# Kernel tuning notes

Measured on AMD Instinct MI355X. Metric: run time of the kernel, lower is better.

The kernel has to match this reference:

```python
import jax, jax.numpy as jnp
import numpy as np

B, S, EMB, H = 2, 2048, 1024, 16
D = EMB // H  # per-head dim = 64
SCALE = 1.0 / np.sqrt(D).astype(np.float32)


def setup_inputs() -> dict:
    key = jax.random.key(0)
    ks = jax.random.split(key, 11)
    lim = 1.0 / np.sqrt(EMB).astype(np.float32)  # torch Linear default init range
    def lin(kw, kb):
        W = jax.random.uniform(kw, (EMB, EMB), jnp.float32, -lim, lim)
        b = jax.random.uniform(kb, (EMB,), jnp.float32, -lim, lim)
        return W, b
    Wq, bq = lin(ks[0], ks[1])
    Wk, bk = lin(ks[2], ks[3])
    Wv, bv = lin(ks[4], ks[5])
    Wo, bo = lin(ks[6], ks[7])
    xq = jax.random.normal(ks[8], (B, S, EMB), jnp.float32)
    xk = jax.random.normal(ks[9], (B, S, EMB), jnp.float32)
    xv = jax.random.normal(ks[10], (B, S, EMB), jnp.float32)
    mask = jnp.tril(jnp.ones((S, S), dtype=jnp.int32))  # causal mask; 0 -> blocked
    return {"xq": xq, "xk": xk, "xv": xv, "mask": mask,
            "Wq": Wq, "bq": bq, "Wk": Wk, "bk": bk,
            "Wv": Wv, "bv": bv, "Wo": Wo, "bo": bo}


def reference(xq, xk, xv, mask, Wq, bq, Wk, bk, Wv, bv, Wo, bo):
    # Projections (torch Linear: x @ W.T + b), then split heads: [B,S,E] -> [B,H,S,D]
    def split_heads(x):
        return x.reshape(B, S, H, D).transpose(0, 2, 1, 3)
    Q = split_heads(xq @ Wq.T + bq)
    K = split_heads(xk @ Wk.T + bk)
    V = split_heads(xv @ Wv.T + bv)
    scores = jnp.einsum("bhqd,bhkd->bhqk", Q, K) * SCALE  # [B,H,S,S]
    scores = jnp.where(mask[None, None, :, :] == 0, jnp.float32(-1e9), scores)
    attn = jax.nn.softmax(scores, axis=-1)  # softmax over key axis (dim=2 per-head in torch)
    res = jnp.einsum("bhqk,bhkd->bhqd", attn, V)
    res = res.transpose(0, 2, 1, 3).reshape(B, S, EMB)  # merge heads back (same slicing layout)
    return res @ Wo.T + bo
```

## Files before the change

kernel.cpp:

```cpp
#include <hip/hip_runtime.h>
#include <hip/hip_bf16.h>

#define BB   2
#define SS   2048
#define EMBD 1024
#define NH   16
#define HD   64
#define QSCALE 0.18033688011112042f
#define NEG_BIG (-1e30f)
#define DEFER_THR 6.0f

typedef __bf16 bf16;
typedef float  floatx4 __attribute__((ext_vector_type(4)));
typedef __bf16 bf16x4  __attribute__((ext_vector_type(4)));
typedef __bf16 bf16x8  __attribute__((ext_vector_type(8)));

typedef const __attribute__((address_space(1))) void* gas_ptr;
typedef __attribute__((address_space(3))) void*       las_ptr;

__device__ __forceinline__ void gl_lds16(const void* g, void* l) {
    __builtin_amdgcn_global_load_lds((gas_ptr)g, (las_ptr)l, 16, 0, 0);
}

__device__ __forceinline__ bf16x8 cvt8(const float* p) {
    bf16x8 o;
#pragma unroll
    for (int j = 0; j < 8; j++) o[j] = (bf16)p[j];
    return o;
}

__global__ __launch_bounds__(256) void cvt_all(
    const float* __restrict__ xq, const float* __restrict__ xk,
    const float* __restrict__ xv, const float* __restrict__ Wq,
    const float* __restrict__ Wk, const float* __restrict__ Wv,
    const float* __restrict__ Wo, bf16* __restrict__ xqo,
    bf16* __restrict__ xko, bf16* __restrict__ xvo, bf16* __restrict__ Wqo,
    bf16* __restrict__ Wko, bf16* __restrict__ Wvo, bf16* __restrict__ Woo) {
    const int y = blockIdx.y;
    const float* src;
    bf16* dst;
    size_t n;
    const size_t NX = (size_t)BB * SS * EMBD;
    const size_t NW = (size_t)EMBD * EMBD;
    switch (y) {
        case 0: src = xq; dst = xqo; n = NX; break;
        case 1: src = xk; dst = xko; n = NX; break;
        case 2: src = xv; dst = xvo; n = NX; break;
        case 3: src = Wq; dst = Wqo; n = NW; break;
        case 4: src = Wk; dst = Wko; n = NW; break;
        case 5: src = Wv; dst = Wvo; n = NW; break;
        default: src = Wo; dst = Woo; n = NW; break;
    }
    const size_t stride = (size_t)gridDim.x * blockDim.x * 4;
    for (size_t i = ((size_t)blockIdx.x * blockDim.x + threadIdx.x) * 4;
         i < n; i += stride) {
        floatx4 v = *(const floatx4*)(src + i);
        bf16x4 o = {(bf16)v[0], (bf16)v[1], (bf16)v[2], (bf16)v[3]};
        *(bf16x4*)(dst + i) = o;
    }
}

extern __shared__ __align__(16) char smem[];

template <int MODE, int FM>
__device__ __forceinline__ void gemm_body(const bf16* __restrict__ A,
                                          const bf16* __restrict__ W,
                                          const float* __restrict__ bias,
                                          void* __restrict__ Ov,
                                          int mBase, int nBase, float oscale) {
    constexpr int BM = 32 * FM;
    constexpr int ABYTES = BM * 64 * 2;
    bf16* As = (bf16*)smem;
    bf16* Bs = (bf16*)(smem + ABYTES);

    const int t = threadIdx.x;
    const int l = t & 63, w = t >> 6;
    const int lm = l & 15, lq = l >> 4;
    const int K = 1024;
    const int wm = (w >> 1) * (16 * FM), wn = (w & 1) * 64;

    const floatx4 zero = {0.f, 0.f, 0.f, 0.f};
    floatx4 acc[FM][4];
#pragma unroll
    for (int i = 0; i < FM; i++)
#pragma unroll
        for (int j = 0; j < 4; j++) acc[i][j] = zero;

    for (int kb = 0; kb < K; kb += 64) {
        __syncthreads();
#pragma unroll
        for (int ia = 0; ia < FM; ia++) {
            int half = ia / (FM / 2 > 0 ? FM / 2 : 1);
            int rem  = (ia % (FM / 2 > 0 ? FM / 2 : 1)) * 256 + t;
            int row  = rem >> 2;
            int col  = half * 32 + (rem & 3) * 8;
            gl_lds16(A + (size_t)(mBase + row) * K + kb + col,
                     (char*)As + (ia * 256 + w * 64) * 16);
        }
#pragma unroll
        for (int i = 0; i < 4; i++) {
            int half = i >> 1;
            int rem  = (i & 1) * 256 + t;
            int row  = rem >> 2;
            int col  = half * 32 + (rem & 3) * 8;
            gl_lds16(W + (size_t)(nBase + row) * K + kb + col,
                     (char*)Bs + (i * 256 + w * 64) * 16);
        }
        __syncthreads();

#pragma unroll
        for (int half = 0; half < 2; half++) {
            const bf16* Ah = As + half * BM * 32;
            const bf16* Bh = Bs + half * 128 * 32;
            bf16x8 af[FM], bfv[4];
#pragma unroll
            for (int f = 0; f < FM; f++)
                af[f] = *(const bf16x8*)&Ah[(wm + f * 16 + lm) * 32 + lq * 8];
#pragma unroll
            for (int f = 0; f < 4; f++)
                bfv[f] = *(const bf16x8*)&Bh[(wn + f * 16 + lm) * 32 + lq * 8];
            if (MODE == 2) {
#pragma unroll
                for (int i = 0; i < 4; i++)
#pragma unroll
                    for (int j = 0; j < FM; j++)
                        acc[j][i] = __builtin_amdgcn_mfma_f32_16x16x32_bf16(
                            bfv[i], af[j], acc[j][i], 0, 0, 0);
            } else {
#pragma unroll
                for (int fm = 0; fm < FM; fm++)
#pragma unroll
                    for (int fn = 0; fn < 4; fn++)
                        acc[fm][fn] =
                            __builtin_amdgcn_mfma_f32_16x16x32_bf16(
                                af[fm], bfv[fn], acc[fm][fn], 0, 0, 0);
            }
        }
    }

    __syncthreads();
    float* rp = (float*)smem + w * (16 * 68);

    if (MODE != 2) {
        float bvv[4];
#pragma unroll
        for (int fn = 0; fn < 4; fn++)
            bvv[fn] = bias[nBase + wn + fn * 16 + lm];
#pragma unroll
        for (int fm = 0; fm < FM; fm++) {
#pragma unroll
            for (int fn = 0; fn < 4; fn++)
#pragma unroll
                for (int r = 0; r < 4; r++)
                    rp[(lq * 4 + r) * 68 + fn * 16 + lm] =
                        (acc[fm][fn][r] + bvv[fn]) * oscale;
            if (MODE == 0) {
                int row2 = l >> 3, col8 = l & 7;
                int h = (nBase + wn) >> 6;
#pragma unroll
                for (int p = 0; p < 2; p++) {
                    int row = p * 8 + row2;
                    int m = mBase + wm + fm * 16 + row;
                    int b = m >> 11, s = m & 2047;
                    bf16x8 o = cvt8(&rp[row * 68 + col8 * 8]);
                    *(bf16x8*)((bf16*)Ov +
                               (((size_t)(b * NH + h)) * SS + s) * HD +
                               col8 * 8) = o;
                }
            } else {
                int c4 = l & 15;
#pragma unroll
                for (int p = 0; p < 4; p++) {
                    int row = p * 4 + (l >> 4);
                    int m = mBase + wm + fm * 16 + row;
                    floatx4 o = *(const floatx4*)&rp[row * 68 + c4 * 4];
                    *(floatx4*)((float*)Ov + (size_t)m * EMBD + nBase + wn +
                                c4 * 4) = o;
                }
            }
        }
    } else {
        const int b = (mBase + wm) >> 11;
        const int sbase = (mBase + wm) & 2047;
#pragma unroll
        for (int i = 0; i < 4; i++) {
            float bv[4];
#pragma unroll
            for (int r = 0; r < 4; r++)
                bv[r] = bias[nBase + wn + i * 16 + lq * 4 + r];
#pragma unroll
            for (int j = 0; j < FM; j++)
#pragma unroll
                for (int r = 0; r < 4; r++)
                    rp[(lq * 4 + r) * 68 + j * 16 + lm] =
                        acc[j][i][r] + bv[r];
            int row2 = l >> 3, col8 = l & 7;
#pragma unroll
            for (int p = 0; p < 2; p++) {
                int row = p * 8 + row2;
                int n = nBase + wn + i * 16 + row;
                int h = n >> 6, d = n & 63;
                bf16x8 o = cvt8(&rp[row * 68 + col8 * 8]);
                *(bf16x8*)((bf16*)Ov +
                           ((size_t)(b * NH + h) * HD + d) * SS + sbase +
                           col8 * 8) = o;
            }
        }
    }
}

__global__ __launch_bounds__(256, 4) void gemm_qkv(
    const bf16* __restrict__ xq, const bf16* __restrict__ xk,
    const bf16* __restrict__ xv, const bf16* __restrict__ Wq,
    const bf16* __restrict__ Wk, const bf16* __restrict__ Wv,
    const float* __restrict__ bq, const float* __restrict__ bk,
    const float* __restrict__ bv, bf16* __restrict__ Qo,
    bf16* __restrict__ Ko, bf16* __restrict__ Vo) {
    const int z = blockIdx.z;
    const int mB = blockIdx.x * 128, nB = blockIdx.y * 128;
    if (z == 0)
        gemm_body<0, 4>(xq, Wq, bq, Qo, mB, nB, QSCALE);
    else if (z == 1)
        gemm_body<0, 4>(xk, Wk, bk, Ko, mB, nB, 1.0f);
    else
        gemm_body<2, 4>(xv, Wv, bv, Vo, mB, nB, 1.0f);
}

__global__ __launch_bounds__(256, 4) void gemm_out(
    const bf16* __restrict__ A, const bf16* __restrict__ W,
    const float* __restrict__ bias, float* __restrict__ O) {
    gemm_body<1, 2>(A, W, bias, O, blockIdx.x * 64, blockIdx.y * 128, 1.0f);
}

__global__ __launch_bounds__(256, 3) void attn_fwd(
    const bf16* __restrict__ Qg, const bf16* __restrict__ Kg,
    const bf16* __restrict__ Vtg, bf16* __restrict__ Oatt) {
    __shared__ __align__(16) bf16 Ksb[2 * 64 * 64];
    __shared__ __align__(16) bf16 VTb[2 * 64 * 64];
    __shared__ __align__(16) bf16 Ps[4][16 * 64];

    const int t = threadIdx.x;
    const int l = t & 63, w = t >> 6;
    const int lm = l & 15, lq = l >> 4;
    const int m7 = lm & 7;
    const int x = blockIdx.x;
    const int i5 = x >> 5;
    const int gq = i5 >> 3, jq = i5 & 7;
    const int qt = (gq == 0) ? jq
                 : (gq == 1) ? 15 - jq
                 : (gq == 2) ? 16 + jq
                             : 31 - jq;
    const int bh = (((x >> 3) & 3) << 3) | (x & 7);
    const size_t kbase = (size_t)bh * SS * HD;
    const size_t vbase = (size_t)bh * HD * SS;
    const int b = bh >> 4, h = bh & 15;
    const floatx4 zero = {0.f, 0.f, 0.f, 0.f};

    const int trow = t >> 3, tsl = t & 7;
    const int cswz = ((tsl ^ (trow & 7)) << 3);
    const bf16* kgp = Kg + kbase + (size_t)trow * HD + cswz;
    const bf16* vgp = Vtg + vbase + (size_t)trow * SS + cswz;
    bf16* ksd = Ksb + t * 8;
    bf16* vtd = VTb + t * 8;

    bf16x8 qa0, qa1;
    {
        const bf16* qp =
            Qg + kbase + (size_t)(qt * 64 + w * 16 + lm) * HD + lq * 8;
        qa0 = *(const bf16x8*)qp;
        qa1 = *(const bf16x8*)(qp + 32);
    }

    float m_i = NEG_BIG;
    float l_part = 0.f;
    floatx4 od[4];
#pragma unroll
    for (int dt = 0; dt < 4; dt++) od[dt] = zero;

    const int qglob = qt * 64 + w * 16 + lm;

    gl_lds16(kgp, ksd);
    gl_lds16(kgp + 2048, ksd + 2048);
    gl_lds16(vgp, vtd);
    gl_lds16(vgp + 32 * SS, vtd + 2048);
    __syncthreads();

    for (int kt = 0; kt <= qt; ++kt) {
        const int cur = kt & 1;
        const bf16* Kc = Ksb + cur * 4096;
        const bf16* Vc = VTb + cur * 4096;
        if (kt < qt) {
            const bf16* kp = kgp + (size_t)(kt + 1) * 4096;
            const bf16* vp = vgp + (size_t)(kt + 1) * 64;
            bf16* kn = ksd + (cur ^ 1) * 4096;
            bf16* vn = vtd + (cur ^ 1) * 4096;
            gl_lds16(kp, kn);
            gl_lds16(kp + 2048, kn + 2048);
            gl_lds16(vp, vn);
            gl_lds16(vp + 32 * SS, vn + 2048);
        }

        floatx4 sc[4];
        __builtin_amdgcn_s_setprio(1);
#pragma unroll
        for (int j0 = 0; j0 < 4; j0++) {
            int rowK = j0 * 16 + lm;
            bf16x8 k0 = *(const bf16x8*)&Kc[rowK * 64 + ((lq ^ m7) << 3)];
            bf16x8 k1 =
                *(const bf16x8*)&Kc[rowK * 64 + (((4 + lq) ^ m7) << 3)];
            floatx4 z = zero;
            z = __builtin_amdgcn_mfma_f32_16x16x32_bf16(k0, qa0, z, 0, 0, 0);
            z = __builtin_amdgcn_mfma_f32_16x16x32_bf16(k1, qa1, z, 0, 0, 0);
            sc[j0] = z;
        }
        __builtin_amdgcn_s_setprio(0);
        if (kt == qt) {
#pragma unroll
            for (int j0 = 0; j0 < 4; j0++)
#pragma unroll
                for (int r = 0; r < 4; r++) {
                    int key = kt * 64 + j0 * 16 + lq * 4 + r;
                    if (key > qglob) sc[j0][r] = NEG_BIG;
                }
        }
        float u0 = fmaxf(fmaxf(sc[0][0], sc[0][1]),
                         fmaxf(sc[0][2], sc[0][3]));
        float u1 = fmaxf(fmaxf(sc[1][0], sc[1][1]),
                         fmaxf(sc[1][2], sc[1][3]));
        float u2 = fmaxf(fmaxf(sc[2][0], sc[2][1]),
                         fmaxf(sc[2][2], sc[2][3]));
        float u3 = fmaxf(fmaxf(sc[3][0], sc[3][1]),
                         fmaxf(sc[3][2], sc[3][3]));
        float mt_loc = fmaxf(fmaxf(u0, u1), fmaxf(u2, u3));
        if (__any(mt_loc > m_i + DEFER_THR)) {
            float mt = fmaxf(mt_loc, __shfl_xor(mt_loc, 16));
            mt = fmaxf(mt, __shfl_xor(mt, 32));
            float mnew = fmaxf(m_i, mt);
            float alpha = __builtin_amdgcn_exp2f(m_i - mnew);
            m_i = mnew;
            l_part *= alpha;
            float a0 = __shfl(alpha, lq * 4 + 0);
            float a1 = __shfl(alpha, lq * 4 + 1);
            float a2 = __shfl(alpha, lq * 4 + 2);
            float a3 = __shfl(alpha, lq * 4 + 3);
#pragma unroll
            for (int dt = 0; dt < 4; dt++) {
                od[dt][0] *= a0;
                od[dt][1] *= a1;
                od[dt][2] *= a2;
                od[dt][3] *= a3;
            }
        }
        float psa0 = 0.f, psa1 = 0.f, psa2 = 0.f, psa3 = 0.f;
#pragma unroll
        for (int j0 = 0; j0 < 4; j0++) {
            float p0 = __builtin_amdgcn_exp2f(sc[j0][0] - m_i);
            float p1 = __builtin_amdgcn_exp2f(sc[j0][1] - m_i);
            float p2 = __builtin_amdgcn_exp2f(sc[j0][2] - m_i);
            float p3 = __builtin_amdgcn_exp2f(sc[j0][3] - m_i);
            sc[j0][0] = p0; sc[j0][1] = p1;
            sc[j0][2] = p2; sc[j0][3] = p3;
            psa0 += p0; psa1 += p1; psa2 += p2; psa3 += p3;
        }
        l_part += (psa0 + psa1) + (psa2 + psa3);
#pragma unroll
        for (int j0l = 0; j0l < 4; j0l++) {
            floatx4 s4 = sc[j0l];
            bf16x4 pk = {(bf16)s4[0], (bf16)s4[1], (bf16)s4[2], (bf16)s4[3]};
            *(bf16x4*)&Ps[w][lm * 64 + ((j0l * 16 + lq * 4) ^ (m7 * 8))] = pk;
        }
        bf16x8 pa0 = *(const bf16x8*)&Ps[w][lm * 64 + ((lq * 8) ^ (m7 * 8))];
        bf16x8 pa1 =
            *(const bf16x8*)&Ps[w][lm * 64 + ((32 + lq * 8) ^ (m7 * 8))];
        __builtin_amdgcn_s_setprio(1);
#pragma unroll
        for (int dt = 0; dt < 4; dt++) {
            int rowD = dt * 16 + lm;
            bf16x8 v0 = *(const bf16x8*)&Vc[rowD * 64 + ((lq ^ m7) << 3)];
            od[dt] = __builtin_amdgcn_mfma_f32_16x16x32_bf16(pa0, v0, od[dt],
                                                             0, 0, 0);
            bf16x8 v1 =
                *(const bf16x8*)&Vc[rowD * 64 + (((4 + lq) ^ m7) << 3)];
            od[dt] = __builtin_amdgcn_mfma_f32_16x16x32_bf16(pa1, v1, od[dt],
                                                             0, 0, 0);
        }
        __builtin_amdgcn_s_setprio(0);
        __syncthreads();
    }

    float l_i = l_part + __shfl_xor(l_part, 16);
    l_i += __shfl_xor(l_i, 32);
    float linv = 1.0f / l_i;
    float lr0 = __shfl(linv, lq * 4 + 0);
    float lr1 = __shfl(linv, lq * 4 + 1);
    float lr2 = __shfl(linv, lq * 4 + 2);
    float lr3 = __shfl(linv, lq * 4 + 3);
    float lr[4] = {lr0, lr1, lr2, lr3};
#pragma unroll
    for (int dt = 0; dt < 4; dt++) {
#pragma unroll
        for (int r = 0; r < 4; r++) {
            int s = qt * 64 + w * 16 + lq * 4 + r;
            float v = od[dt][r] * lr[r];
            Oatt[((size_t)(b * SS + s)) * EMBD + h * HD + dt * 16 + lm] =
                (bf16)v;
        }
    }
}

extern "C" void kernel_launch(void* const* d_in, const int* in_sizes, int n_in,
                              void* d_out, int out_size, void* d_ws,
                              size_t ws_size, hipStream_t stream) {
    const float* xq = (const float*)d_in[0];
    const float* xk = (const float*)d_in[1];
    const float* xv = (const float*)d_in[2];
    const float* Wq = (const float*)d_in[4];
    const float* bq = (const float*)d_in[5];
    const float* Wk = (const float*)d_in[6];
    const float* bk = (const float*)d_in[7];
    const float* Wv = (const float*)d_in[8];
    const float* bv = (const float*)d_in[9];
    const float* Wo = (const float*)d_in[10];
    const float* bo = (const float*)d_in[11];
    float* out = (float*)d_out;

    const size_t NX = (size_t)BB * SS * EMBD;
    const size_t NW = (size_t)EMBD * EMBD;
    bf16* Qw  = (bf16*)d_ws;
    bf16* Kw  = Qw + NX;
    bf16* Vw  = Kw + NX;
    bf16* Aw  = Vw + NX;
    bf16* xqb = Aw + NX;
    bf16* xkb = xqb + NX;
    bf16* xvb = xkb + NX;
    bf16* Wqb = xvb + NX;
    bf16* Wkb = Wqb + NW;
    bf16* Wvb = Wkb + NW;
    bf16* Wob = Wvb + NW;

    cvt_all<<<dim3(1024, 7), 256, 0, stream>>>(xq, xk, xv, Wq, Wk, Wv, Wo,
                                               xqb, xkb, xvb, Wqb, Wkb, Wvb,
                                               Wob);
    gemm_qkv<<<dim3(32, 8, 3), 256, 32768, stream>>>(
        xqb, xkb, xvb, Wqb, Wkb, Wvb, bq, bk, bv, Qw, Kw, Vw);
    attn_fwd<<<dim3(1024), 256, 0, stream>>>(Qw, Kw, Vw, Aw);
    gemm_out<<<dim3(64, 8), 256, 24576, stream>>>(Aw, Wob, bo, out);
}
```

Measured before the change: 225.5 us.

## Switch attention to 32x32x16 MFMA with 2 waves and register-shuffled P

The attention kernel now runs 2 waves per block (128 threads), each handling 32 query rows with 32x32x16 bf16 MFMAs for both QK^T and PV, in place of 4 waves using 16x16x32. The P matrix is repacked into MFMA operand layout with cross-half lane shuffles, removing the per-wave LDS staging buffer and its writes and reads. This aims to reduce LDS traffic and instruction count per tile. In exchange it uses more accumulator registers per thread and has fewer waves per block to hide latency, and the K/V tile loads are spread over fewer threads.

```diff
diff --git a/kernel.cpp b/kernel.cpp
--- a/kernel.cpp
+++ b/kernel.cpp
@@ -11,9 +11,12 @@
 #define DEFER_THR 6.0f
 
 typedef __bf16 bf16;
-typedef float  floatx4 __attribute__((ext_vector_type(4)));
+typedef float  floatx4  __attribute__((ext_vector_type(4)));
+typedef float  floatx16 __attribute__((ext_vector_type(16)));
+typedef __bf16 bf16x2  __attribute__((ext_vector_type(2)));
 typedef __bf16 bf16x4  __attribute__((ext_vector_type(4)));
 typedef __bf16 bf16x8  __attribute__((ext_vector_type(8)));
+typedef unsigned uint4v __attribute__((ext_vector_type(4)));
 
 typedef const __attribute__((address_space(1))) void* gas_ptr;
 typedef __attribute__((address_space(3))) void*       las_ptr;
@@ -27,6 +30,11 @@
 #pragma unroll
     for (int j = 0; j < 8; j++) o[j] = (bf16)p[j];
     return o;
+}
+
+__device__ __forceinline__ unsigned pk2(float a, float b) {
+    bf16x2 v = {(bf16)a, (bf16)b};
+    return __builtin_bit_cast(unsigned, v);
 }
 
 __global__ __launch_bounds__(256) void cvt_all(
@@ -232,17 +240,18 @@
     gemm_body<1, 2>(A, W, bias, O, blockIdx.x * 64, blockIdx.y * 128, 1.0f);
 }
 
-__global__ __launch_bounds__(256, 3) void attn_fwd(
+__global__ __launch_bounds__(128, 3) void attn_fwd(
     const bf16* __restrict__ Qg, const bf16* __restrict__ Kg,
     const bf16* __restrict__ Vtg, bf16* __restrict__ Oatt) {
     __shared__ __align__(16) bf16 Ksb[2 * 64 * 64];
     __shared__ __align__(16) bf16 VTb[2 * 64 * 64];
-    __shared__ __align__(16) bf16 Ps[4][16 * 64];
 
     const int t = threadIdx.x;
     const int l = t & 63, w = t >> 6;
-    const int lm = l & 15, lq = l >> 4;
-    const int m7 = lm & 7;
+    const int hi = l >> 5;
+    const int l32 = l & 31;
+    const int l7 = l & 7;
+    const bool lo = (hi == 0);
     const int x = blockIdx.x;
     const int i5 = x >> 5;
     const int gq = i5 >> 3, jq = i5 & 7;
@@ -254,7 +263,6 @@
     const size_t kbase = (size_t)bh * SS * HD;
     const size_t vbase = (size_t)bh * HD * SS;
     const int b = bh >> 4, h = bh & 15;
-    const floatx4 zero = {0.f, 0.f, 0.f, 0.f};
 
     const int trow = t >> 3, tsl = t & 7;
     const int cswz = ((tsl ^ (trow & 7)) << 3);
@@ -263,26 +271,33 @@
     bf16* ksd = Ksb + t * 8;
     bf16* vtd = VTb + t * 8;
 
-    bf16x8 qa0, qa1;
+    bf16x8 qa[4];
     {
         const bf16* qp =
-            Qg + kbase + (size_t)(qt * 64 + w * 16 + lm) * HD + lq * 8;
-        qa0 = *(const bf16x8*)qp;
-        qa1 = *(const bf16x8*)(qp + 32);
-    }
+            Qg + kbase + (size_t)(qt * 64 + w * 32 + l32) * HD + hi * 8;
+        qa[0] = *(const bf16x8*)qp;
+        qa[1] = *(const bf16x8*)(qp + 16);
+        qa[2] = *(const bf16x8*)(qp + 32);
+        qa[3] = *(const bf16x8*)(qp + 48);
+    }
+
+    int soff[4];
+#pragma unroll
+    for (int f = 0; f < 4; f++) soff[f] = (((f * 2 + hi) ^ l7) << 3);
+
+    const int qglob = qt * 64 + w * 32 + l32;
 
     float m_i = NEG_BIG;
     float l_part = 0.f;
-    floatx4 od[4];
-#pragma unroll
-    for (int dt = 0; dt < 4; dt++) od[dt] = zero;
-
-    const int qglob = qt * 64 + w * 16 + lm;
-
-    gl_lds16(kgp, ksd);
-    gl_lds16(kgp + 2048, ksd + 2048);
-    gl_lds16(vgp, vtd);
-    gl_lds16(vgp + 32 * SS, vtd + 2048);
+    floatx16 od0, od1;
+#pragma unroll
+    for (int i = 0; i < 16; i++) { od0[i] = 0.f; od1[i] = 0.f; }
+
+#pragma unroll
+    for (int i = 0; i < 4; i++) {
+        gl_lds16(kgp + i * 1024, ksd + i * 1024);
+        gl_lds16(vgp + (size_t)i * 16 * SS, vtd + i * 1024);
+    }
     __syncthreads();
 
     for (int kt = 0; kt <= qt; ++kt) {
@@ -294,117 +309,128 @@
             const bf16* vp = vgp + (size_t)(kt + 1) * 64;
             bf16* kn = ksd + (cur ^ 1) * 4096;
             bf16* vn = vtd + (cur ^ 1) * 4096;
-            gl_lds16(kp, kn);
-            gl_lds16(kp + 2048, kn + 2048);
-            gl_lds16(vp, vn);
-            gl_lds16(vp + 32 * SS, vn + 2048);
-        }
-
-        floatx4 sc[4];
+#pragma unroll
+            for (int i = 0; i < 4; i++) {
+                gl_lds16(kp + i * 1024, kn + i * 1024);
+                gl_lds16(vp + (size_t)i * 16 * SS, vn + i * 1024);
+            }
+        }
+
+        floatx16 s0, s1;
+#pragma unroll
+        for (int i = 0; i < 16; i++) { s0[i] = 0.f; s1[i] = 0.f; }
+        const int rA = l32 * 64, rB = rA + 2048;
         __builtin_amdgcn_s_setprio(1);
 #pragma unroll
-        for (int j0 = 0; j0 < 4; j0++) {
-            int rowK = j0 * 16 + lm;
-            bf16x8 k0 = *(const bf16x8*)&Kc[rowK * 64 + ((lq ^ m7) << 3)];
-            bf16x8 k1 =
-                *(const bf16x8*)&Kc[rowK * 64 + (((4 + lq) ^ m7) << 3)];
-            floatx4 z = zero;
-            z = __builtin_amdgcn_mfma_f32_16x16x32_bf16(k0, qa0, z, 0, 0, 0);
-            z = __builtin_amdgcn_mfma_f32_16x16x32_bf16(k1, qa1, z, 0, 0, 0);
-            sc[j0] = z;
+        for (int f = 0; f < 4; f++) {
+            bf16x8 k0 = *(const bf16x8*)&Kc[rA + soff[f]];
+            bf16x8 k1 = *(const bf16x8*)&Kc[rB + soff[f]];
+            s0 = __builtin_amdgcn_mfma_f32_32x32x16_bf16(k0, qa[f], s0,
+                                                         0, 0, 0);
+            s1 = __builtin_amdgcn_mfma_f32_32x32x16_bf16(k1, qa[f], s1,
+                                                         0, 0, 0);
         }
         __builtin_amdgcn_s_setprio(0);
+
         if (kt == qt) {
 #pragma unroll
-            for (int j0 = 0; j0 < 4; j0++)
-#pragma unroll
-                for (int r = 0; r < 4; r++) {
-                    int key = kt * 64 + j0 * 16 + lq * 4 + r;
-                    if (key > qglob) sc[j0][r] = NEG_BIG;
-                }
-        }
-        float u0 = fmaxf(fmaxf(sc[0][0], sc[0][1]),
-                         fmaxf(sc[0][2], sc[0][3]));
-        float u1 = fmaxf(fmaxf(sc[1][0], sc[1][1]),
-                         fmaxf(sc[1][2], sc[1][3]));
-        float u2 = fmaxf(fmaxf(sc[2][0], sc[2][1]),
-                         fmaxf(sc[2][2], sc[2][3]));
-        float u3 = fmaxf(fmaxf(sc[3][0], sc[3][1]),
-                         fmaxf(sc[3][2], sc[3][3]));
-        float mt_loc = fmaxf(fmaxf(u0, u1), fmaxf(u2, u3));
-        if (__any(mt_loc > m_i + DEFER_THR)) {
-            float mt = fmaxf(mt_loc, __shfl_xor(mt_loc, 16));
-            mt = fmaxf(mt, __shfl_xor(mt, 32));
-            float mnew = fmaxf(m_i, mt);
+            for (int r = 0; r < 16; r++) {
+                int key = kt * 64 + (r & 3) + 8 * (r >> 2) + 4 * hi;
+                if (key > qglob) s0[r] = NEG_BIG;
+                if (key + 32 > qglob) s1[r] = NEG_BIG;
+            }
+        }
+
+        float u0 = fmaxf(fmaxf(s0[0], s0[1]), fmaxf(s0[2], s0[3]));
+        float u1 = fmaxf(fmaxf(s0[4], s0[5]), fmaxf(s0[6], s0[7]));
+        float u2 = fmaxf(fmaxf(s0[8], s0[9]), fmaxf(s0[10], s0[11]));
+        float u3 = fmaxf(fmaxf(s0[12], s0[13]), fmaxf(s0[14], s0[15]));
+        float u4 = fmaxf(fmaxf(s1[0], s1[1]), fmaxf(s1[2], s1[3]));
+        float u5 = fmaxf(fmaxf(s1[4], s1[5]), fmaxf(s1[6], s1[7]));
+        float u6 = fmaxf(fmaxf(s1[8], s1[9]), fmaxf(s1[10], s1[11]));
+        float u7 = fmaxf(fmaxf(s1[12], s1[13]), fmaxf(s1[14], s1[15]));
+        float mloc = fmaxf(fmaxf(fmaxf(u0, u1), fmaxf(u2, u3)),
+                           fmaxf(fmaxf(u4, u5), fmaxf(u6, u7)));
+
+        if (__any(mloc > m_i + DEFER_THR)) {
+            float mf = fmaxf(mloc, __shfl_xor(mloc, 32));
+            float mnew = fmaxf(m_i, mf);
             float alpha = __builtin_amdgcn_exp2f(m_i - mnew);
             m_i = mnew;
             l_part *= alpha;
-            float a0 = __shfl(alpha, lq * 4 + 0);
-            float a1 = __shfl(alpha, lq * 4 + 1);
-            float a2 = __shfl(alpha, lq * 4 + 2);
-            float a3 = __shfl(alpha, lq * 4 + 3);
-#pragma unroll
-            for (int dt = 0; dt < 4; dt++) {
-                od[dt][0] *= a0;
-                od[dt][1] *= a1;
-                od[dt][2] *= a2;
-                od[dt][3] *= a3;
-            }
-        }
-        float psa0 = 0.f, psa1 = 0.f, psa2 = 0.f, psa3 = 0.f;
-#pragma unroll
-        for (int j0 = 0; j0 < 4; j0++) {
-            float p0 = __builtin_amdgcn_exp2f(sc[j0][0] - m_i);
-            float p1 = __builtin_amdgcn_exp2f(sc[j0][1] - m_i);
-            float p2 = __builtin_amdgcn_exp2f(sc[j0][2] - m_i);
-            float p3 = __builtin_amdgcn_exp2f(sc[j0][3] - m_i);
-            sc[j0][0] = p0; sc[j0][1] = p1;
-            sc[j0][2] = p2; sc[j0][3] = p3;
-            psa0 += p0; psa1 += p1; psa2 += p2; psa3 += p3;
-        }
-        l_part += (psa0 + psa1) + (psa2 + psa3);
-#pragma unroll
-        for (int j0l = 0; j0l < 4; j0l++) {
-            floatx4 s4 = sc[j0l];
-            bf16x4 pk = {(bf16)s4[0], (bf16)s4[1], (bf16)s4[2], (bf16)s4[3]};
-            *(bf16x4*)&Ps[w][lm * 64 + ((j0l * 16 + lq * 4) ^ (m7 * 8))] = pk;
-        }
-        bf16x8 pa0 = *(const bf16x8*)&Ps[w][lm * 64 + ((lq * 8) ^ (m7 * 8))];
-        bf16x8 pa1 =
-            *(const bf16x8*)&Ps[w][lm * 64 + ((32 + lq * 8) ^ (m7 * 8))];
+#pragma unroll
+            for (int r = 0; r < 16; r++) {
+                int qr = (r & 3) + 8 * (r >> 2) + 4 * hi;
+                float ar = __shfl(alpha, qr);
+                od0[r] *= ar;
+                od1[r] *= ar;
+            }
+        }
+
+        float ps0 = 0.f, ps1 = 0.f, ps2 = 0.f, ps3 = 0.f;
+#pragma unroll
+        for (int i = 0; i < 4; i++) {
+            float a0 = __builtin_amdgcn_exp2f(s0[i * 4 + 0] - m_i);
+            float a1 = __builtin_amdgcn_exp2f(s0[i * 4 + 1] - m_i);
+            float a2 = __builtin_amdgcn_exp2f(s0[i * 4 + 2] - m_i);
+            float a3 = __builtin_amdgcn_exp2f(s0[i * 4 + 3] - m_i);
+            s0[i * 4 + 0] = a0; s0[i * 4 + 1] = a1;
+            s0[i * 4 + 2] = a2; s0[i * 4 + 3] = a3;
+            float b0 = __builtin_amdgcn_exp2f(s1[i * 4 + 0] - m_i);
+            float b1 = __builtin_amdgcn_exp2f(s1[i * 4 + 1] - m_i);
+            float b2 = __builtin_amdgcn_exp2f(s1[i * 4 + 2] - m_i);
+            float b3 = __builtin_amdgcn_exp2f(s1[i * 4 + 3] - m_i);
+            s1[i * 4 + 0] = b0; s1[i * 4 + 1] = b1;
+            s1[i * 4 + 2] = b2; s1[i * 4 + 3] = b3;
+            ps0 += a0 + b0; ps1 += a1 + b1;
+            ps2 += a2 + b2; ps3 += a3 + b3;
+        }
+        l_part += (ps0 + ps1) + (ps2 + ps3);
+
+        bf16x8 pa[4];
+#pragma unroll
+        for (int g = 0; g < 2; g++) {
+            const floatx16& s = g ? s1 : s0;
+            unsigned pA0 = pk2(s[0], s[1]),   pB0 = pk2(s[2], s[3]);
+            unsigned pA1 = pk2(s[4], s[5]),   pB1 = pk2(s[6], s[7]);
+            unsigned pA2 = pk2(s[8], s[9]),   pB2 = pk2(s[10], s[11]);
+            unsigned pA3 = pk2(s[12], s[13]), pB3 = pk2(s[14], s[15]);
+            unsigned xA0 = __shfl_xor(pA0, 32), xB0 = __shfl_xor(pB0, 32);
+            unsigned xA1 = __shfl_xor(pA1, 32), xB1 = __shfl_xor(pB1, 32);
+            unsigned xA2 = __shfl_xor(pA2, 32), xB2 = __shfl_xor(pB2, 32);
+            unsigned xA3 = __shfl_xor(pA3, 32), xB3 = __shfl_xor(pB3, 32);
+            uint4v wa = {lo ? pA0 : xA1, lo ? pB0 : xB1,
+                         lo ? xA0 : pA1, lo ? xB0 : pB1};
+            uint4v wb = {lo ? pA2 : xA3, lo ? pB2 : xB3,
+                         lo ? xA2 : pA3, lo ? xB2 : pB3};
+            pa[g * 2 + 0] = __builtin_bit_cast(bf16x8, wa);
+            pa[g * 2 + 1] = __builtin_bit_cast(bf16x8, wb);
+        }
+
         __builtin_amdgcn_s_setprio(1);
 #pragma unroll
-        for (int dt = 0; dt < 4; dt++) {
-            int rowD = dt * 16 + lm;
-            bf16x8 v0 = *(const bf16x8*)&Vc[rowD * 64 + ((lq ^ m7) << 3)];
-            od[dt] = __builtin_amdgcn_mfma_f32_16x16x32_bf16(pa0, v0, od[dt],
-                                                             0, 0, 0);
-            bf16x8 v1 =
-                *(const bf16x8*)&Vc[rowD * 64 + (((4 + lq) ^ m7) << 3)];
-            od[dt] = __builtin_amdgcn_mfma_f32_16x16x32_bf16(pa1, v1, od[dt],
-                                                             0, 0, 0);
+        for (int ks = 0; ks < 4; ks++) {
+            bf16x8 v0 = *(const bf16x8*)&Vc[rA + soff[ks]];
+            bf16x8 v1 = *(const bf16x8*)&Vc[rB + soff[ks]];
+            od0 = __builtin_amdgcn_mfma_f32_32x32x16_bf16(pa[ks], v0, od0,
+                                                          0, 0, 0);
+            od1 = __builtin_amdgcn_mfma_f32_32x32x16_bf16(pa[ks], v1, od1,
+                                                          0, 0, 0);
         }
         __builtin_amdgcn_s_setprio(0);
         __syncthreads();
     }
 
-    float l_i = l_part + __shfl_xor(l_part, 16);
-    l_i += __shfl_xor(l_i, 32);
-    float linv = 1.0f / l_i;
-    float lr0 = __shfl(linv, lq * 4 + 0);
-    float lr1 = __shfl(linv, lq * 4 + 1);
-    float lr2 = __shfl(linv, lq * 4 + 2);
-    float lr3 = __shfl(linv, lq * 4 + 3);
-    float lr[4] = {lr0, lr1, lr2, lr3};
-#pragma unroll
-    for (int dt = 0; dt < 4; dt++) {
-#pragma unroll
-        for (int r = 0; r < 4; r++) {
-            int s = qt * 64 + w * 16 + lq * 4 + r;
-            float v = od[dt][r] * lr[r];
-            Oatt[((size_t)(b * SS + s)) * EMBD + h * HD + dt * 16 + lm] =
-                (bf16)v;
-        }
+    float l_tot = l_part + __shfl_xor(l_part, 32);
+    float linv = 1.0f / l_tot;
+    const size_t obase =
+        ((size_t)(b * SS + qt * 64 + w * 32)) * EMBD + h * HD + l32;
+#pragma unroll
+    for (int r = 0; r < 16; r++) {
+        int qr = (r & 3) + 8 * (r >> 2) + 4 * hi;
+        float lr = __shfl(linv, qr);
+        Oatt[obase + (size_t)qr * EMBD] = (bf16)(od0[r] * lr);
+        Oatt[obase + (size_t)qr * EMBD + 32] = (bf16)(od1[r] * lr);
     }
 }
 
@@ -443,6 +469,6 @@
                                                Wob);
     gemm_qkv<<<dim3(32, 8, 3), 256, 32768, stream>>>(
         xqb, xkb, xvb, Wqb, Wkb, Wvb, bq, bk, bv, Qw, Kw, Vw);
-    attn_fwd<<<dim3(1024), 256, 0, stream>>>(Qw, Kw, Vw, Aw);
+    attn_fwd<<<dim3(1024), 128, 0, stream>>>(Qw, Kw, Vw, Aw);
     gemm_out<<<dim3(64, 8), 256, 24576, stream>>>(Aw, Wob, bo, out);
 }
```

Result: no change. 226.5 us (+0.5%).
